# Kernel tuning notes

Measured on AMD Instinct MI355X. Metric: run time of the kernel, lower is better.

The kernel has to match this reference:

```python
import jax, jax.numpy as jnp
import numpy as np

NUM_HEADS, HEAD_DIM = 4, 64
BLOCK_SIZE, S = 32, 4
LENGTHS = np.array([2048, 1024, 1536, 512, 2048, 1280, 1792, 768])
MAX_LEN = int(LENGTHS.max())            # 2048
NUM_BLOCKS = MAX_LEN // BLOCK_SIZE      # 64
B = len(LENGTHS)
T = int(LENGTHS.sum())                  # 11008
HIDDEN = NUM_HEADS * HEAD_DIM           # 256
SCALE = HEAD_DIM ** -0.5
INV_SCALE = 1.0 / SCALE
EPS = 1e-6


def setup_inputs() -> dict:
    key = jax.random.key(0)
    ks = jax.random.split(key, 6)
    offsets = np.concatenate([[0], np.cumsum(LENGTHS)]).astype(np.int64)
    batch_ids = np.repeat(np.arange(B), LENGTHS).astype(np.int64)
    pos_ids = np.concatenate([np.arange(l) for l in LENGTHS]).astype(np.int64)
    shp = (T, NUM_HEADS, HEAD_DIM)
    return {
        "q": jax.random.normal(ks[0], shp, jnp.float32),
        "k": jax.random.normal(ks[1], shp, jnp.float32),
        "v": jax.random.normal(ks[2], shp, jnp.float32),
        "u": jax.random.normal(ks[3], shp, jnp.float32),
        "Wg_cmp": jax.random.normal(ks[4], (NUM_HEADS, HEAD_DIM), jnp.float32) * 0.1,
        "Wg_slc": jax.random.normal(ks[5], (NUM_HEADS, HEAD_DIM), jnp.float32) * 0.1,
        "x_offsets": jnp.asarray(offsets),
        "batch_ids": jnp.asarray(batch_ids),
        "pos_ids": jnp.asarray(pos_ids),
    }


def _silu(x):
    return x * jax.nn.sigmoid(x)


def _layer_norm(x):
    # non-affine LayerNorm over last dim, eps=1e-6
    mu = jnp.mean(x, -1, keepdims=True)
    var = jnp.mean(jnp.square(x - mu), -1, keepdims=True)
    return (x - mu) / jnp.sqrt(var + EPS)


def _forward(q, k, v, u, Wg_cmp, Wg_slc, x_offsets, batch_ids, pos_ids):
    # jagged -> padded dense [B, MAX_LEN, H, D]
    pad = lambda x: jnp.zeros((B, MAX_LEN, NUM_HEADS, HEAD_DIM), x.dtype).at[batch_ids, pos_ids].set(x)
    pq, pk, pv = pad(q), pad(k), pad(v)

    # gate model: per-head sigmoid linear gates from padded_q; g_slc is unused
    # by the original forward (the slc kernel never consumes it)
    g_cmp = jax.nn.sigmoid(jnp.einsum('bnhd,hd->bnh', pq, Wg_cmp))
    _g_slc = jax.nn.sigmoid(jnp.einsum('bnhd,hd->bnh', pq, Wg_slc))
    g_cmp_jag = g_cmp[batch_ids, pos_ids]  # [T, H]

    # block-compressed K/V: mean over zero-padded blocks of size BLOCK_SIZE
    k_cmp = pk.reshape(B, NUM_BLOCKS, BLOCK_SIZE, NUM_HEADS, HEAD_DIM).mean(2)
    v_cmp = pv.reshape(B, NUM_BLOCKS, BLOCK_SIZE, NUM_HEADS, HEAD_DIM).mean(2)

    # SiLU-activated block-causal compressed attention
    raw = jnp.einsum('bnhd,bmhd->bnhm', pq, k_cmp) * SCALE  # [B, n, H, m]
    q_blk = jnp.arange(MAX_LEN) // BLOCK_SIZE
    k_blk = jnp.arange(NUM_BLOCKS)
    causal = q_blk[:, None] >= k_blk[None, :]   # [MAX_LEN, NUM_BLOCKS]
    local = q_blk[:, None] == k_blk[None, :]
    p_cmp = jnp.where(causal[None, :, None, :], _silu(raw) * INV_SCALE, 0.0)

    # top-S block selection; local block score forced to 1.0; odd slots
    # duplicated from even slots (as in source)
    sel = jnp.where(local[None, :, None, :], 1.0, p_cmp)
    topk = jax.lax.top_k(sel, S)[1]             # [B, MAX_LEN, H, S]
    topk = topk.at[..., 1::2].set(topk[..., 0::2])
    topk_jag = topk[batch_ids, pos_ids]         # [T, H, S]

    # compressed-branch output, gathered to jagged and gated by g_cmp
    o_cmp = jnp.einsum('bnhm,bmhd->bnhd', p_cmp, v_cmp)[batch_ids, pos_ids]
    o_cmp = o_cmp * g_cmp_jag[:, :, None]       # [T, H, D]

    # selected branch: per-row, per-head gather of S blocks of raw K/V
    seq_start = x_offsets[batch_ids]            # [T]
    head_ix = jnp.arange(NUM_HEADS)[None, :, None]
    o_slc = jnp.zeros_like(q)
    for s in range(S):  # fixed small S, duplicates intentionally double-count
        b_idx = topk_jag[:, :, s]               # [T, H]
        pos_in_seq = b_idx[:, :, None] * BLOCK_SIZE + jnp.arange(BLOCK_SIZE)  # [T,H,BS]
        valid = (b_idx[:, :, None] >= 0) & (pos_in_seq <= pos_ids[:, None, None])
        tgt = jnp.clip(seq_start[:, None, None] + pos_in_seq, 0, T - 1)
        k_g = k[tgt, head_ix]                   # [T, H, BS, D]
        score = jnp.einsum('thd,thbd->thb', q, k_g) * SCALE
        p = jnp.where(valid, _silu(score) * INV_SCALE, 0.0)
        v_g = v[tgt, head_ix]                   # [T, H, BS, D]
        o_slc = o_slc + jnp.einsum('thb,thbd->thd', p, v_g)

    # per-token LayerNorm over hidden, scaled by u, then branch sum
    o_cmp = _layer_norm(o_cmp.reshape(T, HIDDEN)).reshape(T, NUM_HEADS, HEAD_DIM) * u
    o_slc = _layer_norm(o_slc.reshape(T, HIDDEN)).reshape(T, NUM_HEADS, HEAD_DIM) * u
    return (o_cmp + o_slc).reshape(T, HIDDEN)


def reference(q, k, v, u, Wg_cmp, Wg_slc, x_offsets, batch_ids, pos_ids):
    return _forward(q, k, v, u, Wg_cmp, Wg_slc, x_offsets, batch_ids, pos_ids)
```

## Files before the change

kernel.cpp:

```cpp
#include <hip/hip_runtime.h>
#include <math.h>

#define NH 4
#define HD 64
#define HIDDEN 256
#define BS 32
#define NB 64
#define SCALE 0.125f
#define INV_SCALE 8.0f

__device__ __forceinline__ float fast_sigmoid(float x) {
    return 1.0f / (1.0f + __expf(-x));
}
__device__ __forceinline__ float readlane_f(float v, int lane) {
    return __int_as_float(__builtin_amdgcn_readlane(__float_as_int(v), lane));
}

__global__ __launch_bounds__(256) void kcmp_kernel(
    const float* __restrict__ k, const float* __restrict__ v,
    const int* __restrict__ x_offsets,
    double* __restrict__ k_cmp, float* __restrict__ v_cmp2) {
    int bb  = blockIdx.x;
    int b   = bb >> 6;
    int blk = bb & 63;
    int tid = threadIdx.x;
    int s0   = x_offsets[b];
    int len  = x_offsets[b + 1] - s0;
    int nblk = len >> 5;
    int h = tid >> 6, d = tid & 63;
    if (blockIdx.y == 0) {
        double acc = 0.0;
        if (blk < nblk) {
            const float* kp = k + (size_t)(s0 + blk * BS) * HIDDEN + tid;
            #pragma unroll
            for (int i = 0; i < BS; ++i) acc += (double)kp[i * HIDDEN];
            acc *= (1.0 / BS);
        }
        k_cmp[((size_t)(b * NH + h) * 64 + blk) * 64 + d] = acc;
    } else {
        float acc = 0.f;
        if (blk < nblk) {
            const float* vp = v + (size_t)(s0 + blk * BS) * HIDDEN + tid;
            #pragma unroll
            for (int i = 0; i < BS; ++i) acc += vp[i * HIDDEN];
            acc *= (1.0f / BS);
        }
        v_cmp2[((size_t)(b * NH + h) * 32 + (blk >> 1)) * 128 + d * 2 + (blk & 1)] = acc;
    }
}

__global__ __launch_bounds__(256, 3) void cmp_kernel(
    const float* __restrict__ q,
    const int* __restrict__ batch_ids, const int* __restrict__ pos_ids,
    const double* __restrict__ k_cmp, const float* __restrict__ v_cmp2,
    float* __restrict__ oc_buf, int2* __restrict__ idxbuf, int T) {
    int t0   = blockIdx.x * 64;
    int h    = blockIdx.y;
    int tid  = threadIdx.x;
    int wv   = __builtin_amdgcn_readfirstlane(tid >> 6);
    int lane = tid & 63;
    int b    = batch_ids[t0];
    int pos0 = pos_ids[t0];

    __shared__ __align__(16) char smem[49920];
    float* qs = (float*)smem;
    float* ps = qs + 64 * 65;
    float* vs = ps + 64 * 66;
    unsigned long long* trip = (unsigned long long*)qs;

    const float* qg = q + (size_t)t0 * HIDDEN + h * HD;
    #pragma unroll
    for (int i = 0; i < 16; ++i) {
        int idx = tid + 256 * i;
        int tok = idx >> 6, dd = idx & 63;
        qs[dd * 65 + tok] = qg[(size_t)tok * HIDDEN + dd];
    }
    const float* vg = v_cmp2 + (size_t)(b * NH + h) * 4096;
    #pragma unroll
    for (int i = 0; i < 16; ++i) vs[tid + 256 * i] = vg[tid + 256 * i];
    __syncthreads();

    int qblk_max = (pos0 + 63) >> 5;
    int m_need   = qblk_max + 2;
    if (m_need > 63) m_need = 63;

    unsigned long long a0 = 0ull, a1 = 0ull, a2 = 0ull;
    if (16 * wv <= m_need) {
        double qd[64];
        #pragma unroll
        for (int dd = 0; dd < 64; ++dd) qd[dd] = (double)qs[dd * 65 + lane];
        int myqblk = (pos0 + lane) >> 5;

        const double* kcb = k_cmp + ((size_t)(b * NH + h) * 64 + wv * 16) * 64;
        #pragma unroll
        for (int mi = 0; mi < 16; ++mi) {
            int m = wv * 16 + mi;
            const double* kr = kcb + mi * 64;
            double accA = 0.0, accB = 0.0;
            #pragma unroll
            for (int dd = 0; dd < 32; ++dd) {
                accA += qd[2 * dd]     * kr[2 * dd];
                accB += qd[2 * dd + 1] * kr[2 * dd + 1];
            }
            double r = (accA + accB) * 0.125;
            double p64 = 0.0;
            if (m <= myqblk) p64 = r / (1.0 + exp(-r)) * 8.0;
            double selv = (m == myqblk) ? 1.0 : p64;
            ps[lane * 66 + m] = (float)p64;
            long long sb = __double_as_longlong(selv);
            unsigned long long kk = (unsigned long long)sb;
            kk = (sb < 0) ? ~kk : (kk | 0x8000000000000000ull);
            kk = (kk & ~63ull) | (unsigned long long)(63 - m);
            if (kk > a0)      { a2 = a1; a1 = a0; a0 = kk; }
            else if (kk > a1) { a2 = a1; a1 = kk; }
            else if (kk > a2) { a2 = kk; }
        }
    }
    __syncthreads();
    trip[(wv * 64 + lane) * 3 + 0] = a0;
    trip[(wv * 64 + lane) * 3 + 1] = a1;
    trip[(wv * 64 + lane) * 3 + 2] = a2;
    __syncthreads();

    if (wv == 0) {
        unsigned long long kk2[4][3];
        #pragma unroll
        for (int w = 0; w < 4; ++w)
            #pragma unroll
            for (int j = 0; j < 3; ++j)
                kk2[w][j] = trip[(w * 64 + lane) * 3 + j];
        int pp[4] = {0, 0, 0, 0};
        int outi[3];
        #pragma unroll
        for (int s = 0; s < 3; ++s) {
            unsigned long long best = 0ull; int bw = 0;
            #pragma unroll
            for (int w = 0; w < 4; ++w) {
                unsigned long long hd_ = (pp[w] == 0) ? kk2[w][0]
                                       : (pp[w] == 1) ? kk2[w][1] : kk2[w][2];
                if (hd_ > best) { best = hd_; bw = w; }
            }
            outi[s] = 63 - (int)(best & 63ull);
            #pragma unroll
            for (int w = 0; w < 4; ++w) if (w == bw) pp[w]++;
        }
        idxbuf[(size_t)(t0 + lane) * NH + h] = make_int2(outi[0], outi[2]);
    }

    float occ[16];
    #pragma unroll
    for (int tt = 0; tt < 16; ++tt) occ[tt] = 0.f;
    int mmax2 = qblk_max >> 1;
    const float2* vs2 = (const float2*)vs;
    for (int m2 = 0; m2 <= mmax2; ++m2) {
        float2 vv = vs2[m2 * 64 + lane];
        #pragma unroll
        for (int tt = 0; tt < 16; ++tt) {
            int tok = wv * 16 + tt;
            float2 pv = *(const float2*)(ps + tok * 66 + 2 * m2);
            occ[tt] += pv.x * vv.x + pv.y * vv.y;
        }
    }
    #pragma unroll
    for (int tt = 0; tt < 16; ++tt)
        oc_buf[(size_t)(t0 + wv * 16 + tt) * HIDDEN + h * HD + lane] = occ[tt];
}

__global__ __launch_bounds__(256) void slc_kernel(
    const float* __restrict__ q, const float* __restrict__ k,
    const float* __restrict__ v,
    const int* __restrict__ x_offsets, const int* __restrict__ batch_ids,
    const int* __restrict__ pos_ids,
    const int2* __restrict__ idxbuf, float* __restrict__ os_out, int T) {
    int i  = blockIdx.x;
    int wg = (i & 7) * (gridDim.x >> 3) + (i >> 3);
    int qb = wg >> 2;
    int h  = wg & 3;
    int t0 = qb * 32;
    int tid  = threadIdx.x;
    int wv   = __builtin_amdgcn_readfirstlane(tid >> 6);
    int lane = tid & 63;

    int b    = batch_ids[t0];
    int pos0 = pos_ids[t0];
    int s0   = x_offsets[b];
    int qblk = pos0 >> 5;

    __shared__ float q_lds[32 * 68];
    __shared__ float os_lds[32 * 64];
    __shared__ float vs_lds[4 * 32 * 64];
    float* vs_w = vs_lds + wv * 2048;

    const float4* q4 = (const float4*)(q + (size_t)t0 * HIDDEN + h * HD);
    #pragma unroll
    for (int rep = 0; rep < 2; ++rep) {
        int f4i = tid + 256 * rep;
        int tk = f4i >> 4, c4 = f4i & 15;
        *(float4*)(&q_lds[tk * 68 + c4 * 4]) = q4[(size_t)tk * 64 + c4];
    }
    #pragma unroll
    for (int rep = 0; rep < 8; ++rep) os_lds[tid + 256 * rep] = 0.f;

    int myi0 = -1, myi2 = -1;
    unsigned long long U = 0ull;
    if (lane < 32) {
        int2 ix = idxbuf[(size_t)(t0 + lane) * NH + h];
        myi0 = ix.x;
        myi2 = (ix.y <= qblk) ? ix.y : -1;
        U = (1ull << myi0);
        if (myi2 >= 0) U |= (1ull << myi2);
    }
    #pragma unroll
    for (int off = 1; off < 64; off <<= 1) U |= __shfl_xor(U, off, 64);
    __syncthreads();

    int r  = lane & 15, cc = lane >> 4;
    const float* kbase = k + (size_t)s0 * HIDDEN + h * HD;
    const float* vbase = v + (size_t)s0 * HIDDEN + h * HD + lane;

    int cnt = 0;
    while (U) {
        int m = (int)__builtin_ctzll(U); U &= U - 1;
        if (((cnt++) & 3) != wv) continue;
        const float* kb_p = kbase + (size_t)(m * BS) * HIDDEN;
        float4 kb0[4], kb1[4];
        #pragma unroll
        for (int j = 0; j < 4; ++j) {
            kb0[j] = *(const float4*)(kb_p + (size_t)r * HIDDEN + (cc + 4 * j) * 4);
            kb1[j] = *(const float4*)(kb_p + (size_t)(16 + r) * HIDDEN + (cc + 4 * j) * 4);
        }
        {
            const float* vb_p = vbase + (size_t)(m * BS) * HIDDEN;
            #pragma unroll
            for (int g = 0; g < 4; ++g) {
                const float* p0_ = vb_p + (size_t)(g * 8) * HIDDEN;
                float x0 = p0_[0 * HIDDEN], x1 = p0_[1 * HIDDEN];
                float x2 = p0_[2 * HIDDEN], x3 = p0_[3 * HIDDEN];
                float x4 = p0_[4 * HIDDEN], x5 = p0_[5 * HIDDEN];
                float x6 = p0_[6 * HIDDEN], x7 = p0_[7 * HIDDEN];
                float* d0 = vs_w + (g * 8) * 64 + lane;
                d0[0 * 64] = x0; d0[1 * 64] = x1; d0[2 * 64] = x2; d0[3 * 64] = x3;
                d0[4 * 64] = x4; d0[5 * 64] = x5; d0[6 * 64] = x6; d0[7 * 64] = x7;
            }
        }
        #pragma unroll
        for (int j = 0; j < 4; ++j) {
            asm volatile("" : "+v"(kb0[j].x), "+v"(kb0[j].y),
                              "+v"(kb0[j].z), "+v"(kb0[j].w));
            asm volatile("" : "+v"(kb1[j].x), "+v"(kb1[j].y),
                              "+v"(kb1[j].z), "+v"(kb1[j].w));
        }

        unsigned long long want =
            __ballot(lane < 32 && (myi0 == m || myi2 == m));
        while (want) {
            int tk = (int)__builtin_ctzll(want); want &= want - 1;
            int pos_tk = pos0 + tk;
            const float* qrow = &q_lds[tk * 68];
            float psA0 = 0.f, psB0 = 0.f, psA1 = 0.f, psB1 = 0.f;
            #pragma unroll
            for (int j = 0; j < 4; ++j) {
                float4 qq = *(const float4*)(qrow + (cc + 4 * j) * 4);
                if (j & 1) {
                    psB0 += qq.x * kb0[j].x + qq.y * kb0[j].y
                          + qq.z * kb0[j].z + qq.w * kb0[j].w;
                    psB1 += qq.x * kb1[j].x + qq.y * kb1[j].y
                          + qq.z * kb1[j].z + qq.w * kb1[j].w;
                } else {
                    psA0 += qq.x * kb0[j].x + qq.y * kb0[j].y
                          + qq.z * kb0[j].z + qq.w * kb0[j].w;
                    psA1 += qq.x * kb1[j].x + qq.y * kb1[j].y
                          + qq.z * kb1[j].z + qq.w * kb1[j].w;
                }
            }
            float psum0 = psA0 + psB0, psum1 = psA1 + psB1;
            psum0 += __shfl_xor(psum0, 16, 64); psum0 += __shfl_xor(psum0, 32, 64);
            psum1 += __shfl_xor(psum1, 16, 64); psum1 += __shfl_xor(psum1, 32, 64);
            float scv0 = psum0 * SCALE, scv1 = psum1 * SCALE;
            int row0 = m * BS + r;
            float p0 = (row0 <= pos_tk)      ? scv0 * fast_sigmoid(scv0) * 16.f : 0.f;
            float p1 = (row0 + 16 <= pos_tk) ? scv1 * fast_sigmoid(scv1) * 16.f : 0.f;
            float ostA = 0.f, ostB = 0.f;
            #pragma unroll
            for (int rr = 0; rr < 16; ++rr) {
                ostA += readlane_f(p0, rr) * vs_w[rr * 64 + lane];
                ostB += readlane_f(p1, rr) * vs_w[(16 + rr) * 64 + lane];
            }
            atomicAdd(&os_lds[tk * 64 + lane], ostA + ostB);
        }
    }
    __syncthreads();

    float* ob = os_out + (size_t)t0 * HIDDEN + h * HD;
    #pragma unroll
    for (int rep = 0; rep < 8; ++rep) {
        int idx = tid + 256 * rep;
        int tk = idx >> 6, d = idx & 63;
        ob[(size_t)tk * HIDDEN + d] = os_lds[idx];
    }
}

__global__ __launch_bounds__(256) void ln_kernel(
    const float* __restrict__ q, const float* __restrict__ u,
    const float* __restrict__ Wg_cmp,
    const float* __restrict__ oc_buf, float* __restrict__ io, int T) {
    int tid = threadIdx.x;
    int grp = tid >> 5;
    int sub = tid & 31;
    int t   = blockIdx.x * 8 + grp;
    int D0  = sub * 8;

    const float4* qp = (const float4*)(q + (size_t)t * HIDDEN + D0);
    float4 qa = qp[0], qb = qp[1];
    const float4* wp = (const float4*)(Wg_cmp + D0);
    float4 wa = wp[0], wb = wp[1];
    float gp = qa.x * wa.x + qa.y * wa.y + qa.z * wa.z + qa.w * wa.w
             + qb.x * wb.x + qb.y * wb.y + qb.z * wb.z + qb.w * wb.w;
    gp += __shfl_xor(gp, 1, 64);
    gp += __shfl_xor(gp, 2, 64);
    gp += __shfl_xor(gp, 4, 64);
    float g = fast_sigmoid(gp);

    const float4* ocp = (const float4*)(oc_buf + (size_t)t * HIDDEN + D0);
    float4 oa = ocp[0], ob = ocp[1];
    oa.x *= g; oa.y *= g; oa.z *= g; oa.w *= g;
    ob.x *= g; ob.y *= g; ob.z *= g; ob.w *= g;
    float4* iop = (float4*)(io + (size_t)t * HIDDEN + D0);
    float4 sa = iop[0], sb = iop[1];

    float sc_ = oa.x + oa.y + oa.z + oa.w + ob.x + ob.y + ob.z + ob.w;
    float sc2 = oa.x * oa.x + oa.y * oa.y + oa.z * oa.z + oa.w * oa.w
              + ob.x * ob.x + ob.y * ob.y + ob.z * ob.z + ob.w * ob.w;
    float ss_ = sa.x + sa.y + sa.z + sa.w + sb.x + sb.y + sb.z + sb.w;
    float ss2 = sa.x * sa.x + sa.y * sa.y + sa.z * sa.z + sa.w * sa.w
              + sb.x * sb.x + sb.y * sb.y + sb.z * sb.z + sb.w * sb.w;
    #pragma unroll
    for (int off = 1; off < 32; off <<= 1) {
        sc_ += __shfl_xor(sc_, off, 64);
        sc2 += __shfl_xor(sc2, off, 64);
        ss_ += __shfl_xor(ss_, off, 64);
        ss2 += __shfl_xor(ss2, off, 64);
    }
    float muc  = sc_ * (1.0f / HIDDEN);
    float varc = sc2 * (1.0f / HIDDEN) - muc * muc;
    float mus  = ss_ * (1.0f / HIDDEN);
    float vars = ss2 * (1.0f / HIDDEN) - mus * mus;
    float rc = rsqrtf(varc + 1e-6f), rs = rsqrtf(vars + 1e-6f);

    const float4* up = (const float4*)(u + (size_t)t * HIDDEN + D0);
    float4 ua = up[0], ub = up[1];
    float4 o0, o1;
    o0.x = ((oa.x - muc) * rc + (sa.x - mus) * rs) * ua.x;
    o0.y = ((oa.y - muc) * rc + (sa.y - mus) * rs) * ua.y;
    o0.z = ((oa.z - muc) * rc + (sa.z - mus) * rs) * ua.z;
    o0.w = ((oa.w - muc) * rc + (sa.w - mus) * rs) * ua.w;
    o1.x = ((ob.x - muc) * rc + (sb.x - mus) * rs) * ub.x;
    o1.y = ((ob.y - muc) * rc + (sb.y - mus) * rs) * ub.y;
    o1.z = ((ob.z - muc) * rc + (sb.z - mus) * rs) * ub.z;
    o1.w = ((ob.w - muc) * rc + (sb.w - mus) * rs) * ub.w;
    iop[0] = o0; iop[1] = o1;
}

extern "C" void kernel_launch(void* const* d_in, const int* in_sizes, int n_in,
                              void* d_out, int out_size, void* d_ws, size_t ws_size,
                              hipStream_t stream) {
    const float* q      = (const float*)d_in[0];
    const float* k      = (const float*)d_in[1];
    const float* v      = (const float*)d_in[2];
    const float* u      = (const float*)d_in[3];
    const float* Wg_cmp = (const float*)d_in[4];
    const int* x_offsets = (const int*)d_in[6];
    const int* batch_ids = (const int*)d_in[7];
    const int* pos_ids   = (const int*)d_in[8];

    int T = in_sizes[0] / HIDDEN;
    int B = in_sizes[6] - 1;

    double* k_cmp  = (double*)d_ws;
    float*  v_cmp2 = (float*)(k_cmp + (size_t)B * NH * 4096);
    float*  oc_buf = v_cmp2 + (size_t)B * NH * 4096;
    int2*   idxbuf = (int2*)(oc_buf + (size_t)T * HIDDEN);

    kcmp_kernel<<<dim3(B * NB, 2), 256, 0, stream>>>(k, v, x_offsets, k_cmp, v_cmp2);
    cmp_kernel<<<dim3(T / 64, NH), 256, 0, stream>>>(
        q, batch_ids, pos_ids, k_cmp, v_cmp2, oc_buf, idxbuf, T);
    slc_kernel<<<dim3((T / 32) * NH), 256, 0, stream>>>(
        q, k, v, x_offsets, batch_ids, pos_ids, idxbuf, (float*)d_out, T);
    ln_kernel<<<dim3(T / 8), 256, 0, stream>>>(
        q, u, Wg_cmp, oc_buf, (float*)d_out, T);
}
```

Baseline: 210.8 us.

## Split selected-attention into work-list build and per-block single-wave kernels

Replaces the slc kernel, which gave each query-block/head one workgroup with four waves sharing the selected KV blocks, with two kernels. A build kernel zeroes the output and writes a compact list of (KV block, token mask) entries per query block and head. A second kernel launches one 64-thread wave per possible entry, exits early on unused slots, and atomically adds into global output. It also processes two tokens per iteration so the V reads from LDS are shared. The aim is better load balance and more parallelism, at the cost of an extra launch, many empty waves, global atomics, and q reads straight from global memory.

```diff
diff --git a/kernel.cpp b/kernel.cpp
--- a/kernel.cpp
+++ b/kernel.cpp
@@ -166,40 +166,22 @@
         oc_buf[(size_t)(t0 + wv * 16 + tt) * HIDDEN + h * HD + lane] = occ[tt];
 }
 
-__global__ __launch_bounds__(256) void slc_kernel(
-    const float* __restrict__ q, const float* __restrict__ k,
-    const float* __restrict__ v,
-    const int* __restrict__ x_offsets, const int* __restrict__ batch_ids,
-    const int* __restrict__ pos_ids,
-    const int2* __restrict__ idxbuf, float* __restrict__ os_out, int T) {
-    int i  = blockIdx.x;
-    int wg = (i & 7) * (gridDim.x >> 3) + (i >> 3);
-    int qb = wg >> 2;
-    int h  = wg & 3;
-    int t0 = qb * 32;
-    int tid  = threadIdx.x;
-    int wv   = __builtin_amdgcn_readfirstlane(tid >> 6);
-    int lane = tid & 63;
-
-    int b    = batch_ids[t0];
+__global__ __launch_bounds__(64) void build_kernel(
+    const int* __restrict__ pos_ids, const int2* __restrict__ idxbuf,
+    int* __restrict__ cnt_arr, int2* __restrict__ entries,
+    float* __restrict__ os_out, int T) {
+    int wg   = blockIdx.x;
+    int qb   = wg >> 2;
+    int h    = wg & 3;
+    int t0   = qb * 32;
+    int lane = threadIdx.x;
+
     int pos0 = pos_ids[t0];
-    int s0   = x_offsets[b];
     int qblk = pos0 >> 5;
 
-    __shared__ float q_lds[32 * 68];
-    __shared__ float os_lds[32 * 64];
-    __shared__ float vs_lds[4 * 32 * 64];
-    float* vs_w = vs_lds + wv * 2048;
-
-    const float4* q4 = (const float4*)(q + (size_t)t0 * HIDDEN + h * HD);
-    #pragma unroll
-    for (int rep = 0; rep < 2; ++rep) {
-        int f4i = tid + 256 * rep;
-        int tk = f4i >> 4, c4 = f4i & 15;
-        *(float4*)(&q_lds[tk * 68 + c4 * 4]) = q4[(size_t)tk * 64 + c4];
-    }
-    #pragma unroll
-    for (int rep = 0; rep < 8; ++rep) os_lds[tid + 256 * rep] = 0.f;
+    float* ob = os_out + (size_t)t0 * HIDDEN + h * HD + lane;
+    #pragma unroll
+    for (int tk = 0; tk < 32; ++tk) ob[(size_t)tk * HIDDEN] = 0.f;
 
     int myi0 = -1, myi2 = -1;
     unsigned long long U = 0ull;
@@ -212,91 +194,146 @@
     }
     #pragma unroll
     for (int off = 1; off < 64; off <<= 1) U |= __shfl_xor(U, off, 64);
-    __syncthreads();
-
-    int r  = lane & 15, cc = lane >> 4;
-    const float* kbase = k + (size_t)s0 * HIDDEN + h * HD;
-    const float* vbase = v + (size_t)s0 * HIDDEN + h * HD + lane;
-
-    int cnt = 0;
+
+    int slot = 0;
     while (U) {
         int m = (int)__builtin_ctzll(U); U &= U - 1;
-        if (((cnt++) & 3) != wv) continue;
-        const float* kb_p = kbase + (size_t)(m * BS) * HIDDEN;
-        float4 kb0[4], kb1[4];
-        #pragma unroll
-        for (int j = 0; j < 4; ++j) {
-            kb0[j] = *(const float4*)(kb_p + (size_t)r * HIDDEN + (cc + 4 * j) * 4);
-            kb1[j] = *(const float4*)(kb_p + (size_t)(16 + r) * HIDDEN + (cc + 4 * j) * 4);
-        }
+        unsigned long long wm = __ballot(lane < 32 && (myi0 == m || myi2 == m));
+        if (lane == 0) entries[(size_t)wg * 64 + slot] = make_int2(m, (int)wm);
+        slot++;
+    }
+    if (lane == 0) cnt_arr[wg] = slot;
+}
+
+__global__ __launch_bounds__(64, 4) void slc2_kernel(
+    const float* __restrict__ q, const float* __restrict__ k,
+    const float* __restrict__ v,
+    const int* __restrict__ x_offsets, const int* __restrict__ batch_ids,
+    const int* __restrict__ pos_ids,
+    const int* __restrict__ cnt_arr, const int2* __restrict__ entries,
+    float* __restrict__ os_out, int T) {
+    int i  = blockIdx.x;
+    int wgidx = (i & 7) * (gridDim.x >> 3) + (i >> 3);
+    int slot = wgidx & 63;
+    int wg   = wgidx >> 6;
+    if (slot >= cnt_arr[wg]) return;
+
+    int2 e = entries[(size_t)wg * 64 + slot];
+    int m = e.x;
+    unsigned int want = (unsigned int)e.y;
+    int qb = wg >> 2, h = wg & 3;
+    int t0 = qb * 32;
+    int lane = threadIdx.x;
+    int r = lane & 15, cc = lane >> 4;
+
+    int pos0 = pos_ids[t0];
+    int s0   = x_offsets[batch_ids[t0]];
+
+    __shared__ float vs_w[32 * 64];
+
+    const float* kb_p = k + (size_t)(s0 + m * BS) * HIDDEN + h * HD;
+    float4 kb0[4], kb1[4];
+    #pragma unroll
+    for (int j = 0; j < 4; ++j) {
+        kb0[j] = *(const float4*)(kb_p + (size_t)r * HIDDEN + (cc + 4 * j) * 4);
+        kb1[j] = *(const float4*)(kb_p + (size_t)(16 + r) * HIDDEN + (cc + 4 * j) * 4);
+    }
+    {
+        const float* vb_p = v + (size_t)(s0 + m * BS) * HIDDEN + h * HD + lane;
+        #pragma unroll
+        for (int g = 0; g < 4; ++g) {
+            const float* p0_ = vb_p + (size_t)(g * 8) * HIDDEN;
+            float x0 = p0_[0 * HIDDEN], x1 = p0_[1 * HIDDEN];
+            float x2 = p0_[2 * HIDDEN], x3 = p0_[3 * HIDDEN];
+            float x4 = p0_[4 * HIDDEN], x5 = p0_[5 * HIDDEN];
+            float x6 = p0_[6 * HIDDEN], x7 = p0_[7 * HIDDEN];
+            float* d0 = vs_w + (g * 8) * 64 + lane;
+            d0[0 * 64] = x0; d0[1 * 64] = x1; d0[2 * 64] = x2; d0[3 * 64] = x3;
+            d0[4 * 64] = x4; d0[5 * 64] = x5; d0[6 * 64] = x6; d0[7 * 64] = x7;
+        }
+    }
+    #pragma unroll
+    for (int j = 0; j < 4; ++j) {
+        asm volatile("" : "+v"(kb0[j].x), "+v"(kb0[j].y),
+                          "+v"(kb0[j].z), "+v"(kb0[j].w));
+        asm volatile("" : "+v"(kb1[j].x), "+v"(kb1[j].y),
+                          "+v"(kb1[j].z), "+v"(kb1[j].w));
+    }
+    int row0 = m * BS + r;
+
+    while (want) {
+        int tk0 = (int)__builtin_ctz(want); want &= want - 1;
+        int tk1 = -1;
+        if (want) { tk1 = (int)__builtin_ctz(want); want &= want - 1; }
+
+        const float4* qr0 = (const float4*)(q + (size_t)(t0 + tk0) * HIDDEN + h * HD);
+        const float4* qr1 = (tk1 >= 0)
+            ? (const float4*)(q + (size_t)(t0 + tk1) * HIDDEN + h * HD) : qr0;
+        float4 qa[4], qb[4];
+        #pragma unroll
+        for (int j = 0; j < 4; ++j) { qa[j] = qr0[cc + 4 * j]; qb[j] = qr1[cc + 4 * j]; }
+
+        float pa0, pa1, pb0 = 0.f, pb1 = 0.f;
         {
-            const float* vb_p = vbase + (size_t)(m * BS) * HIDDEN;
-            #pragma unroll
-            for (int g = 0; g < 4; ++g) {
-                const float* p0_ = vb_p + (size_t)(g * 8) * HIDDEN;
-                float x0 = p0_[0 * HIDDEN], x1 = p0_[1 * HIDDEN];
-                float x2 = p0_[2 * HIDDEN], x3 = p0_[3 * HIDDEN];
-                float x4 = p0_[4 * HIDDEN], x5 = p0_[5 * HIDDEN];
-                float x6 = p0_[6 * HIDDEN], x7 = p0_[7 * HIDDEN];
-                float* d0 = vs_w + (g * 8) * 64 + lane;
-                d0[0 * 64] = x0; d0[1 * 64] = x1; d0[2 * 64] = x2; d0[3 * 64] = x3;
-                d0[4 * 64] = x4; d0[5 * 64] = x5; d0[6 * 64] = x6; d0[7 * 64] = x7;
-            }
-        }
-        #pragma unroll
-        for (int j = 0; j < 4; ++j) {
-            asm volatile("" : "+v"(kb0[j].x), "+v"(kb0[j].y),
-                              "+v"(kb0[j].z), "+v"(kb0[j].w));
-            asm volatile("" : "+v"(kb1[j].x), "+v"(kb1[j].y),
-                              "+v"(kb1[j].z), "+v"(kb1[j].w));
-        }
-
-        unsigned long long want =
-            __ballot(lane < 32 && (myi0 == m || myi2 == m));
-        while (want) {
-            int tk = (int)__builtin_ctzll(want); want &= want - 1;
-            int pos_tk = pos0 + tk;
-            const float* qrow = &q_lds[tk * 68];
+            int pos_tk = pos0 + tk0;
             float psA0 = 0.f, psB0 = 0.f, psA1 = 0.f, psB1 = 0.f;
             #pragma unroll
             for (int j = 0; j < 4; ++j) {
-                float4 qq = *(const float4*)(qrow + (cc + 4 * j) * 4);
                 if (j & 1) {
-                    psB0 += qq.x * kb0[j].x + qq.y * kb0[j].y
-                          + qq.z * kb0[j].z + qq.w * kb0[j].w;
-                    psB1 += qq.x * kb1[j].x + qq.y * kb1[j].y
-                          + qq.z * kb1[j].z + qq.w * kb1[j].w;
+                    psB0 += qa[j].x * kb0[j].x + qa[j].y * kb0[j].y
+                          + qa[j].z * kb0[j].z + qa[j].w * kb0[j].w;
+                    psB1 += qa[j].x * kb1[j].x + qa[j].y * kb1[j].y
+                          + qa[j].z * kb1[j].z + qa[j].w * kb1[j].w;
                 } else {
-                    psA0 += qq.x * kb0[j].x + qq.y * kb0[j].y
-                          + qq.z * kb0[j].z + qq.w * kb0[j].w;
-                    psA1 += qq.x * kb1[j].x + qq.y * kb1[j].y
-                          + qq.z * kb1[j].z + qq.w * kb1[j].w;
+                    psA0 += qa[j].x * kb0[j].x + qa[j].y * kb0[j].y
+                          + qa[j].z * kb0[j].z + qa[j].w * kb0[j].w;
+                    psA1 += qa[j].x * kb1[j].x + qa[j].y * kb1[j].y
+                          + qa[j].z * kb1[j].z + qa[j].w * kb1[j].w;
                 }
             }
             float psum0 = psA0 + psB0, psum1 = psA1 + psB1;
             psum0 += __shfl_xor(psum0, 16, 64); psum0 += __shfl_xor(psum0, 32, 64);
             psum1 += __shfl_xor(psum1, 16, 64); psum1 += __shfl_xor(psum1, 32, 64);
             float scv0 = psum0 * SCALE, scv1 = psum1 * SCALE;
-            int row0 = m * BS + r;
-            float p0 = (row0 <= pos_tk)      ? scv0 * fast_sigmoid(scv0) * 16.f : 0.f;
-            float p1 = (row0 + 16 <= pos_tk) ? scv1 * fast_sigmoid(scv1) * 16.f : 0.f;
-            float ostA = 0.f, ostB = 0.f;
-            #pragma unroll
-            for (int rr = 0; rr < 16; ++rr) {
-                ostA += readlane_f(p0, rr) * vs_w[rr * 64 + lane];
-                ostB += readlane_f(p1, rr) * vs_w[(16 + rr) * 64 + lane];
+            pa0 = (row0 <= pos_tk)      ? scv0 * fast_sigmoid(scv0) * 16.f : 0.f;
+            pa1 = (row0 + 16 <= pos_tk) ? scv1 * fast_sigmoid(scv1) * 16.f : 0.f;
+        }
+        if (tk1 >= 0) {
+            int pos_tk = pos0 + tk1;
+            float psA0 = 0.f, psB0 = 0.f, psA1 = 0.f, psB1 = 0.f;
+            #pragma unroll
+            for (int j = 0; j < 4; ++j) {
+                if (j & 1) {
+                    psB0 += qb[j].x * kb0[j].x + qb[j].y * kb0[j].y
+                          + qb[j].z * kb0[j].z + qb[j].w * kb0[j].w;
+                    psB1 += qb[j].x * kb1[j].x + qb[j].y * kb1[j].y
+                          + qb[j].z * kb1[j].z + qb[j].w * kb1[j].w;
+                } else {
+                    psA0 += qb[j].x * kb0[j].x + qb[j].y * kb0[j].y
+                          + qb[j].z * kb0[j].z + qb[j].w * kb0[j].w;
+                    psA1 += qb[j].x * kb1[j].x + qb[j].y * kb1[j].y
+                          + qb[j].z * kb1[j].z + qb[j].w * kb1[j].w;
+                }
             }
-            atomicAdd(&os_lds[tk * 64 + lane], ostA + ostB);
-        }
-    }
-    __syncthreads();
-
-    float* ob = os_out + (size_t)t0 * HIDDEN + h * HD;
-    #pragma unroll
-    for (int rep = 0; rep < 8; ++rep) {
-        int idx = tid + 256 * rep;
-        int tk = idx >> 6, d = idx & 63;
-        ob[(size_t)tk * HIDDEN + d] = os_lds[idx];
+            float psum0 = psA0 + psB0, psum1 = psA1 + psB1;
+            psum0 += __shfl_xor(psum0, 16, 64); psum0 += __shfl_xor(psum0, 32, 64);
+            psum1 += __shfl_xor(psum1, 16, 64); psum1 += __shfl_xor(psum1, 32, 64);
+            float scv0 = psum0 * SCALE, scv1 = psum1 * SCALE;
+            pb0 = (row0 <= pos_tk)      ? scv0 * fast_sigmoid(scv0) * 16.f : 0.f;
+            pb1 = (row0 + 16 <= pos_tk) ? scv1 * fast_sigmoid(scv1) * 16.f : 0.f;
+        }
+
+        float oA0 = 0.f, oA1 = 0.f, oB0 = 0.f, oB1 = 0.f;
+        #pragma unroll
+        for (int rr = 0; rr < 16; ++rr) {
+            float v0 = vs_w[rr * 64 + lane];
+            float v1 = vs_w[(16 + rr) * 64 + lane];
+            oA0 += readlane_f(pa0, rr) * v0;  oA1 += readlane_f(pa1, rr) * v1;
+            oB0 += readlane_f(pb0, rr) * v0;  oB1 += readlane_f(pb1, rr) * v1;
+        }
+        atomicAdd(&os_out[(size_t)(t0 + tk0) * HIDDEN + h * HD + lane], oA0 + oA1);
+        if (tk1 >= 0)
+            atomicAdd(&os_out[(size_t)(t0 + tk1) * HIDDEN + h * HD + lane], oB0 + oB1);
     }
 }
 
@@ -380,12 +417,19 @@
     float*  v_cmp2 = (float*)(k_cmp + (size_t)B * NH * 4096);
     float*  oc_buf = v_cmp2 + (size_t)B * NH * 4096;
     int2*   idxbuf = (int2*)(oc_buf + (size_t)T * HIDDEN);
+    int2*   entries = idxbuf + (size_t)T * NH;
+    int*    cnt_arr = (int*)(entries + (size_t)(T / 32) * NH * 64);
+
+    int nwg = (T / 32) * NH;
 
     kcmp_kernel<<<dim3(B * NB, 2), 256, 0, stream>>>(k, v, x_offsets, k_cmp, v_cmp2);
     cmp_kernel<<<dim3(T / 64, NH), 256, 0, stream>>>(
         q, batch_ids, pos_ids, k_cmp, v_cmp2, oc_buf, idxbuf, T);
-    slc_kernel<<<dim3((T / 32) * NH), 256, 0, stream>>>(
-        q, k, v, x_offsets, batch_ids, pos_ids, idxbuf, (float*)d_out, T);
+    build_kernel<<<dim3(nwg), 64, 0, stream>>>(
+        pos_ids, idxbuf, cnt_arr, entries, (float*)d_out, T);
+    slc2_kernel<<<dim3(nwg * 64), 64, 0, stream>>>(
+        q, k, v, x_offsets, batch_ids, pos_ids, cnt_arr, entries,
+        (float*)d_out, T);
     ln_kernel<<<dim3(T / 8), 256, 0, stream>>>(
         q, u, Wg_cmp, oc_buf, (float*)d_out, T);
 }
```

Measured after the change: 208.3 us. About the same (-1.2%).
